# Kernel optimization log

Measured on AMD Instinct MI355X. Metric: run time of the kernel, lower is better.

The kernel has to match this reference:

```python
import jax, jax.numpy as jnp
import numpy as np

WET_MIX = 0.3
FEEDBACK = 0.4
ROOM_SIZE = 0.5
NUM_REFL = 8
NUM_HEADS = 4

# Delay kernel table: int(delay) in {0,1,2,>=3} -> kernel_size {identity,3,5,7}.
# A k-tap kernel with padding k//2 == the same kernel zero-padded to 7 taps with padding 3.
def _gauss7(ks):
    g = np.exp(-np.linspace(-2.0, 2.0, ks) ** 2)
    g = g / g.sum()
    out = np.zeros(7, np.float32)
    s = (7 - ks) // 2
    out[s:s + ks] = g
    return out
_delta = np.zeros(7, np.float32); _delta[3] = 1.0
K_TABLE = jnp.asarray(np.stack([_delta, _gauss7(3), _gauss7(5), _gauss7(7)]))  # [4,7]


def _conv2d(x, w, b, pad):
    y = jax.lax.conv_general_dilated(x, w, (1, 1), [(pad, pad), (pad, pad)],
                                     dimension_numbers=('NCHW', 'OIHW', 'NCHW'))
    return y + b[None, :, None, None]


def _delay_line(x, kern7):
    # vertical depthwise Gaussian blur, same for every (batch, channel) plane
    b, c, h, w = x.shape
    k = kern7.reshape(1, 1, 7, 1)
    y = jax.lax.conv_general_dilated(x.reshape(b * c, 1, h, w), k, (1, 1), [(3, 3), (0, 0)],
                                     dimension_numbers=('NCHW', 'OIHW', 'NCHW'))
    return y.reshape(b, c, h, w)


def _forward(x, refl_w, refl_d, sc_w, sc_b, fb_w, fb_b, d1_w, d1_b, d2_w, d2_b,
             in_proj_w, in_proj_b, out_proj_w, out_proj_b, oc_w, oc_b):
    B, C, H, W = x.shape
    scaled = refl_d * ROOM_SIZE
    kidx = jnp.clip(jnp.floor(scaled).astype(jnp.int32), 0, 3)  # int(delay) detaches grad, as in torch

    wet = jnp.zeros_like(x)
    fb_buf = x * 0.1
    spatial = _conv2d(x, sc_w, sc_b, 1)  # [B,2C,H,W]

    for i in range(NUM_REFL):
        refl = _delay_line(fb_buf, K_TABLE[kidx[i]])
        refl = _conv2d(refl, fb_w, fb_b, 1)
        damp = jax.nn.sigmoid(_conv2d(jax.nn.silu(_conv2d(refl, d1_w, d1_b, 0)), d2_w, d2_b, 0))
        refl = refl * damp
        weight = jax.nn.sigmoid(refl_w[i]) * (0.8 ** i)
        wet = wet + refl * weight
        fb_buf = fb_buf + refl * (FEEDBACK * 0.1)

    # MultiheadAttention over L = H*W tokens, embed_dim=C=4, 4 heads (head_dim=1)
    L = H * W
    hd = C // NUM_HEADS
    wet_flat = wet.reshape(B, C, L).transpose(0, 2, 1)           # [B,L,C]
    qkv = wet_flat @ in_proj_w.T + in_proj_b                     # [B,L,3C]
    q, k, v = jnp.split(qkv, 3, axis=-1)
    def heads(t):
        return t.reshape(B, L, NUM_HEADS, hd).transpose(0, 2, 1, 3)  # [B,H,L,hd]
    q, k, v = heads(q), heads(k), heads(v)
    scores = jnp.einsum('bhqd,bhkd->bhqk', q, k) / np.sqrt(hd).astype(np.float32)
    attn = jax.nn.softmax(scores, axis=-1)
    o = jnp.einsum('bhqk,bhkd->bhqd', attn, v)
    o = o.transpose(0, 2, 1, 3).reshape(B, L, C) @ out_proj_w.T + out_proj_b
    wet2 = o.transpose(0, 2, 1).reshape(B, C, H, W)

    combined = jnp.concatenate([spatial, wet2], axis=1)          # [B,3C,H,W]
    processed_wet = _conv2d(combined, oc_w, oc_b, 0)
    return x * (1.0 - WET_MIX) + processed_wet * WET_MIX


def setup_inputs() -> dict:
    key = jax.random.key(0)
    ks = jax.random.split(key, 16)
    B, C, H, W = 2, 4, 64, 64
    f32 = jnp.float32
    return {
        'x': jax.random.normal(ks[0], (B, C, H, W), f32),
        'refl_w': jax.random.normal(ks[1], (8,), f32) * 0.1,
        'refl_d': jax.random.randint(ks[2], (8,), 1, 16).astype(f32),
        'sc_w': jax.random.normal(ks[3], (2 * C, C, 3, 3), f32) * 0.1,
        'sc_b': jnp.zeros((2 * C,), f32),
        'fb_w': jax.random.normal(ks[4], (C, C, 3, 3), f32) * 0.1,
        'fb_b': jnp.zeros((C,), f32),
        'd1_w': jax.random.normal(ks[5], (C // 2, C, 1, 1), f32) * 0.3,
        'd1_b': jnp.zeros((C // 2,), f32),
        'd2_w': jax.random.normal(ks[6], (C, C // 2, 1, 1), f32) * 0.3,
        'd2_b': jnp.zeros((C,), f32),
        'in_proj_w': jax.random.normal(ks[7], (3 * C, C), f32) * 0.3,
        'in_proj_b': jnp.zeros((3 * C,), f32),
        'out_proj_w': jax.random.normal(ks[8], (C, C), f32) * 0.3,
        'out_proj_b': jnp.zeros((C,), f32),
        'oc_w': jax.random.normal(ks[9], (C, 3 * C, 1, 1), f32) * 0.2,
        'oc_b': jnp.zeros((C,), f32),
    }


def reference(x, refl_w, refl_d, sc_w, sc_b, fb_w, fb_b, d1_w, d1_b, d2_w, d2_b,
              in_proj_w, in_proj_b, out_proj_w, out_proj_b, oc_w, oc_b):
    return _forward(x, refl_w, refl_d, sc_w, sc_b, fb_w, fb_b, d1_w, d1_b, d2_w, d2_b,
                    in_proj_w, in_proj_b, out_proj_w, out_proj_b, oc_w, oc_b)
```

## Files before the change

### kernel.cpp

```cpp
#include <hip/hip_runtime.h>
#include <math.h>


#define ZERO4 make_float4(0.f, 0.f, 0.f, 0.f)

__device__ __forceinline__ float sigf(float v) { return 1.0f / (1.0f + __expf(-v)); }

__device__ __forceinline__ float dppL(float v) {
    return __int_as_float(__builtin_amdgcn_mov_dpp(__float_as_int(v), 0x138, 0xf, 0xf, true));
}
__device__ __forceinline__ float dppR(float v) {
    return __int_as_float(__builtin_amdgcn_mov_dpp(__float_as_int(v), 0x130, 0xf, 0xf, true));
}
__device__ __forceinline__ float4 shL4(float4 v) {
    return make_float4(dppL(v.x), dppL(v.y), dppL(v.z), dppL(v.w));
}
__device__ __forceinline__ float4 shR4(float4 v) {
    return make_float4(dppR(v.x), dppR(v.y), dppR(v.z), dppR(v.w));
}

__device__ __forceinline__ void tapL(float4& a, const float4 t, const float4* w) {
    const float4 w0 = w[0], w1 = w[1], w2 = w[2], w3 = w[3];
    a.x += w0.x * t.x + w1.x * t.y + w2.x * t.z + w3.x * t.w;
    a.y += w0.y * t.x + w1.y * t.y + w2.y * t.z + w3.y * t.w;
    a.z += w0.z * t.x + w1.z * t.y + w2.z * t.z + w3.z * t.w;
    a.w += w0.w * t.x + w1.w * t.y + w2.w * t.z + w3.w * t.w;
}

__global__ __launch_bounds__(1024, 1) void reverb_qkv_kernel(
    const float* __restrict__ x,
    const float* __restrict__ refl_w,
    const float* __restrict__ refl_d,
    const float* __restrict__ fb_w,
    const float* __restrict__ fb_b,
    const float* __restrict__ d1_w,
    const float* __restrict__ d1_b,
    const float* __restrict__ d2_w,
    const float* __restrict__ d2_b,
    const float* __restrict__ ipw,
    const float* __restrict__ ipb,
    float* __restrict__ Qg, float* __restrict__ Kg, float* __restrict__ Vg)
{
    __shared__ float4 P [17 * 64];
    __shared__ float4 BL[17 * 64];
    __shared__ float4 WT[64];
    __shared__ float  GT[3][8];
    __shared__ float  WL[9 * 16];

    const int blk   = blockIdx.x;
    const int batch = blk >> 6;
    const int c0    = blk & 63;
    const int LB    = c0 - 8;
    const int tid   = threadIdx.x;
    const int wy    = tid >> 6;
    const int r     = tid & 63;

    if (tid < 3) {
        const int rr = tid + 1;
        const int ks = 2 * rr + 1;
        const int s  = (7 - ks) >> 1;
        const double step = 4.0 / (double)(ks - 1);
        double g[7]; double sum = 0.0;
        for (int t = 0; t < 7; ++t) {
            if (t < ks) { double u = -2.0 + step * (double)t; g[t] = exp(-u * u); sum += g[t]; }
        }
        for (int t = 0; t < 7; ++t) GT[tid][t] = 0.0f;
        for (int t = 0; t < ks; ++t) GT[tid][s + t] = (float)(g[t] / sum);
    }
    if (tid >= 64 && tid < 64 + 144) {
        const int idx = tid - 64;
        const int oc  = idx / 36;
        const int rem = idx - oc * 36;
        const int ic  = rem / 9;
        const int tp  = rem - ic * 9;
        WL[tp * 16 + ic * 4 + oc] = fb_w[idx];
    }

    for (int idx = tid; idx < 17 * 64; idx += 1024) {
        const int lc  = idx >> 6;
        const int row = idx & 63;
        const int gc  = LB + lc;
        float4 v = ZERO4;
        if (gc >= 0 && gc < 64) {
            const int base = batch * 16384 + row * 64 + gc;
            v.x = 0.1f * x[base];
            v.y = 0.1f * x[base + 4096];
            v.z = 0.1f * x[base + 8192];
            v.w = 0.1f * x[base + 12288];
        }
        P[idx] = v;
    }
    __syncthreads();

    const float4* WL4 = (const float4*)WL;

    double w8 = 1.0;
    for (int j = 0; j < 8; ++j) {
        int kidx = (int)floorf(refl_d[j] * 0.5f);
        kidx = kidx < 0 ? 0 : (kidx > 3 ? 3 : kidx);
        float kv[7];
        #pragma unroll
        for (int u = 0; u < 7; ++u) {
            const float dv = (u == 3) ? 1.0f : 0.0f;
            kv[u] = (kidx == 0) ? dv : GT[kidx - 1][u];
        }
        const float wgt = sigf(refl_w[j]) * (float)w8;

        const int rad = 7 - j;
        const int clo = max(0, c0 - rad);
        const int chi = min(64, c0 + 1 + rad);

        const int lcA   = (clo - 1) - LB;
        const int nBlur = (chi + 1) - (clo - 1);
        for (int t = wy; t < nBlur; t += 16) {
            const int lc = lcA + t;
            const int gc = LB + lc;
            float4 b = ZERO4;
            if (gc >= 0 && gc < 64) {
                const float4 v  = P[lc * 64 + r];
                const float4 l1 = shL4(v),  l2 = shL4(l1), l3 = shL4(l2);
                const float4 r1 = shR4(v),  r2 = shR4(r1), r3 = shR4(r2);
                b.x = kv[0]*l3.x + kv[1]*l2.x + kv[2]*l1.x + kv[3]*v.x
                    + kv[4]*r1.x + kv[5]*r2.x + kv[6]*r3.x;
                b.y = kv[0]*l3.y + kv[1]*l2.y + kv[2]*l1.y + kv[3]*v.y
                    + kv[4]*r1.y + kv[5]*r2.y + kv[6]*r3.y;
                b.z = kv[0]*l3.z + kv[1]*l2.z + kv[2]*l1.z + kv[3]*v.z
                    + kv[4]*r1.z + kv[5]*r2.z + kv[6]*r3.z;
                b.w = kv[0]*l3.w + kv[1]*l2.w + kv[2]*l1.w + kv[3]*v.w
                    + kv[4]*r1.w + kv[5]*r2.w + kv[6]*r3.w;
            }
            BL[lc * 64 + r] = b;
        }
        __syncthreads();

        const int c = clo + wy;
        if (wy < chi - clo) {
            const int lc = c - LB;
            const float4 bm = BL[(lc - 1) * 64 + r];
            const float4 bc = BL[lc * 64 + r];
            const float4 bp = BL[(lc + 1) * 64 + r];

            float4 acc = make_float4(fb_b[0], fb_b[1], fb_b[2], fb_b[3]);
            tapL(acc, shL4(bm), WL4 + 0*4);  tapL(acc, shL4(bc), WL4 + 1*4);  tapL(acc, shL4(bp), WL4 + 2*4);
            tapL(acc, bm,       WL4 + 3*4);  tapL(acc, bc,       WL4 + 4*4);  tapL(acc, bp,       WL4 + 5*4);
            tapL(acc, shR4(bm), WL4 + 6*4);  tapL(acc, shR4(bc), WL4 + 7*4);  tapL(acc, shR4(bp), WL4 + 8*4);

            float4 rr = acc;
            float h0 = d1_b[0] + d1_w[0]*rr.x + d1_w[1]*rr.y + d1_w[2]*rr.z + d1_w[3]*rr.w;
            float h1 = d1_b[1] + d1_w[4]*rr.x + d1_w[5]*rr.y + d1_w[6]*rr.z + d1_w[7]*rr.w;
            h0 = h0 * sigf(h0);
            h1 = h1 * sigf(h1);
            const float d0  = sigf(d2_b[0] + d2_w[0]*h0 + d2_w[1]*h1);
            const float d1v = sigf(d2_b[1] + d2_w[2]*h0 + d2_w[3]*h1);
            const float d2v = sigf(d2_b[2] + d2_w[4]*h0 + d2_w[5]*h1);
            const float d3v = sigf(d2_b[3] + d2_w[6]*h0 + d2_w[7]*h1);
            rr.x *= d0; rr.y *= d1v; rr.z *= d2v; rr.w *= d3v;

            const float4 oldfb = P[lc * 64 + r];
            P[lc * 64 + r] = make_float4(oldfb.x + 0.04f*rr.x, oldfb.y + 0.04f*rr.y,
                                         oldfb.z + 0.04f*rr.z, oldfb.w + 0.04f*rr.w);

            if (c == c0) {
                float4 wv = make_float4(wgt*rr.x, wgt*rr.y, wgt*rr.z, wgt*rr.w);
                if (j > 0) {
                    const float4 old = WT[r];
                    wv.x += old.x; wv.y += old.y; wv.z += old.z; wv.w += old.w;
                }
                WT[r] = wv;
            }
        }
        __syncthreads();
        w8 *= 0.8;
    }

    if (tid < 64) {
        const float4 wv = WT[tid];
        #pragma unroll
        for (int h = 0; h < 4; ++h) {
            const float q = ipb[h]
                + ipw[h*4+0]*wv.x + ipw[h*4+1]*wv.y
                + ipw[h*4+2]*wv.z + ipw[h*4+3]*wv.w;
            const float k = ipb[4+h]
                + ipw[(4+h)*4+0]*wv.x + ipw[(4+h)*4+1]*wv.y
                + ipw[(4+h)*4+2]*wv.z + ipw[(4+h)*4+3]*wv.w;
            const float v = ipb[8+h]
                + ipw[(8+h)*4+0]*wv.x + ipw[(8+h)*4+1]*wv.y
                + ipw[(8+h)*4+2]*wv.z + ipw[(8+h)*4+3]*wv.w;
            const int o = (batch * 4 + h) * 4096 + tid * 64 + c0;
            Qg[o] = q; Kg[o] = k; Vg[o] = v;
        }
    }
}

__global__ __launch_bounds__(512) void attn_kernel(
    const float* __restrict__ Qg, const float* __restrict__ Kg,
    const float* __restrict__ Vg,
    float* __restrict__ PN, float* __restrict__ PD, float* __restrict__ PM)
{
    __shared__ float2 KV[1024];
    __shared__ float  wred[16];
    __shared__ float  pN[4][512], pD[4][512];

    const int bh  = blockIdx.x >> 6;
    const int sub = (blockIdx.x >> 2) & 15;
    const int ks  = blockIdx.x & 3;
    const int tid = threadIdx.x;

    const float* Kp = Kg + bh * 4096 + ks * 1024;
    const float* Vp = Vg + bh * 4096 + ks * 1024;

    float pmax = -3.0e38f, pmin = 3.0e38f;
    #pragma unroll
    for (int t = tid; t < 1024; t += 512) {
        const float kk = Kp[t];
        const float vv = Vp[t];
        KV[t] = make_float2(kk, vv);
        pmax = fmaxf(pmax, kk);
        pmin = fminf(pmin, kk);
    }
    #pragma unroll
    for (int off = 32; off > 0; off >>= 1) {
        pmax = fmaxf(pmax, __shfl_xor(pmax, off, 64));
        pmin = fminf(pmin, __shfl_xor(pmin, off, 64));
    }
    if ((tid & 63) == 0) { wred[tid >> 6] = pmax; wred[8 + (tid >> 6)] = pmin; }
    __syncthreads();
    float kmax = wred[0], kmin = wred[8];
    #pragma unroll
    for (int w = 1; w < 8; ++w) {
        kmax = fmaxf(kmax, wred[w]);
        kmin = fminf(kmin, wred[8 + w]);
    }

    const int ql = tid & 63;
    const int kh = __builtin_amdgcn_readfirstlane(tid >> 6);

    const float L2E = 1.4426950408889634f;
    float q2[4], nm2[4];
    #pragma unroll
    for (int t = 0; t < 4; ++t) {
        const float q = Qg[bh * 4096 + sub * 256 + ql + 64 * t];
        q2[t]  = q * L2E;
        nm2[t] = -(((q >= 0.0f) ? q * kmax : q * kmin) * L2E);
    }

    const float4* KV4 = (const float4*)KV;
    const int base4 = kh * 64;

    float num[4] = {0.f, 0.f, 0.f, 0.f};
    float den[4] = {0.f, 0.f, 0.f, 0.f};
    #pragma unroll 8
    for (int j = 0; j < 64; ++j) {
        const float4 f = KV4[base4 + j];
        #pragma unroll
        for (int t = 0; t < 4; ++t) {
            const float e0 = __builtin_amdgcn_exp2f(__fmaf_rn(q2[t], f.x, nm2[t]));
            den[t] += e0;  num[t] = __fmaf_rn(e0, f.y, num[t]);
            const float e1 = __builtin_amdgcn_exp2f(__fmaf_rn(q2[t], f.z, nm2[t]));
            den[t] += e1;  num[t] = __fmaf_rn(e1, f.w, num[t]);
        }
    }
    #pragma unroll
    for (int t = 0; t < 4; ++t) {
        pN[t][tid] = num[t];
        pD[t][tid] = den[t];
    }
    __syncthreads();
    if (tid < 256) {
        const int which = tid >> 6;
        const int qa    = tid & 63;
        float n = 0.f, d = 0.f;
        #pragma unroll
        for (int w = 0; w < 8; ++w) {
            n += pN[which][w * 64 + qa];
            d += pD[which][w * 64 + qa];
        }
        const int qi = sub * 256 + tid;
        const int o  = bh * 16384 + ks * 4096 + qi;
        PN[o] = n;
        PD[o] = d;
        const float q = Qg[bh * 4096 + qi];
        PM[o] = ((q >= 0.0f) ? q * kmax : q * kmin) * L2E;
    }
}

__global__ __launch_bounds__(128) void final_kernel(
    const float* __restrict__ x,
    const float* __restrict__ sc_w, const float* __restrict__ sc_b,
    const float* __restrict__ opw,  const float* __restrict__ opb,
    const float* __restrict__ ocw,  const float* __restrict__ ocb,
    const float* __restrict__ PN,   const float* __restrict__ PD,
    const float* __restrict__ PM,   float* __restrict__ out)
{
    const int g   = blockIdx.x * 128 + threadIdx.x;
    const int b   = g >> 12;
    const int pix = g & 4095;
    const int y   = pix >> 6;
    const int xc  = pix & 63;

    float xin[4][3][3];
    #pragma unroll
    for (int ic = 0; ic < 4; ++ic)
        #pragma unroll
        for (int ky = 0; ky < 3; ++ky)
            #pragma unroll
            for (int kx = 0; kx < 3; ++kx) {
                const int yy = y + ky - 1, xx = xc + kx - 1;
                xin[ic][ky][kx] = (yy >= 0 && yy < 64 && xx >= 0 && xx < 64)
                                    ? x[(b * 4 + ic) * 4096 + yy * 64 + xx] : 0.f;
            }

    float sp[8];
    #pragma unroll
    for (int oc = 0; oc < 8; ++oc) {
        float a = sc_b[oc];
        #pragma unroll
        for (int ic = 0; ic < 4; ++ic)
            #pragma unroll
            for (int ky = 0; ky < 3; ++ky)
                #pragma unroll
                for (int kx = 0; kx < 3; ++kx)
                    a += sc_w[(oc * 4 + ic) * 9 + ky * 3 + kx] * xin[ic][ky][kx];
        sp[oc] = a;
    }

    float oh[4];
    #pragma unroll
    for (int h = 0; h < 4; ++h) {
        const int bh = b * 4 + h;
        float m2s[4];
        #pragma unroll
        for (int ks = 0; ks < 4; ++ks) m2s[ks] = PM[bh * 16384 + ks * 4096 + pix];
        const float M2 = fmaxf(fmaxf(m2s[0], m2s[1]), fmaxf(m2s[2], m2s[3]));
        float n = 0.f, d = 0.f;
        #pragma unroll
        for (int ks = 0; ks < 4; ++ks) {
            const float s = __builtin_amdgcn_exp2f(m2s[ks] - M2);
            n = __fmaf_rn(PN[bh * 16384 + ks * 4096 + pix], s, n);
            d = __fmaf_rn(PD[bh * 16384 + ks * 4096 + pix], s, d);
        }
        oh[h] = n / d;
    }

    float w2[4];
    #pragma unroll
    for (int c = 0; c < 4; ++c)
        w2[c] = opb[c] + opw[c*4+0]*oh[0] + opw[c*4+1]*oh[1]
                       + opw[c*4+2]*oh[2] + opw[c*4+3]*oh[3];

    #pragma unroll
    for (int c = 0; c < 4; ++c) {
        float a = ocb[c];
        #pragma unroll
        for (int j = 0; j < 8; ++j) a += ocw[c * 12 + j] * sp[j];
        #pragma unroll
        for (int h = 0; h < 4; ++h) a += ocw[c * 12 + 8 + h] * w2[h];
        const int idx = (b * 4 + c) * 4096 + y * 64 + xc;
        out[idx] = 0.7f * x[idx] + 0.3f * a;
    }
}

extern "C" void kernel_launch(void* const* d_in, const int* in_sizes, int n_in,
                              void* d_out, int out_size, void* d_ws, size_t ws_size,
                              hipStream_t stream) {
    const float* x      = (const float*)d_in[0];
    const float* refl_w = (const float*)d_in[1];
    const float* refl_d = (const float*)d_in[2];
    const float* sc_w   = (const float*)d_in[3];
    const float* sc_b   = (const float*)d_in[4];
    const float* fb_w   = (const float*)d_in[5];
    const float* fb_b   = (const float*)d_in[6];
    const float* d1_w   = (const float*)d_in[7];
    const float* d1_b   = (const float*)d_in[8];
    const float* d2_w   = (const float*)d_in[9];
    const float* d2_b   = (const float*)d_in[10];
    const float* ipw    = (const float*)d_in[11];
    const float* ipb    = (const float*)d_in[12];
    const float* opw    = (const float*)d_in[13];
    const float* opb    = (const float*)d_in[14];
    const float* ocw    = (const float*)d_in[15];
    const float* ocb    = (const float*)d_in[16];
    float* out = (float*)d_out;

    float* Q  = (float*)d_ws;
    float* K  = Q + 32768;
    float* V  = K + 32768;
    float* PN = V + 32768;
    float* PD = PN + 131072;
    float* PM = PD + 131072;

    reverb_qkv_kernel<<<dim3(128), dim3(1024), 0, stream>>>(
        x, refl_w, refl_d, fb_w, fb_b, d1_w, d1_b, d2_w, d2_b, ipw, ipb,
        Q, K, V);
    attn_kernel<<<dim3(512), dim3(512), 0, stream>>>(Q, K, V, PN, PD, PM);
    final_kernel<<<dim3(64), dim3(128), 0, stream>>>(
        x, sc_w, sc_b, opw, opb, ocw, ocb, PN, PD, PM, out);
}
```

Baseline: 130.8 us.

## Fuse three kernels into one persistent kernel with grid barriers

```diff
diff --git a/kernel.cpp b/kernel.cpp
--- a/kernel.cpp
+++ b/kernel.cpp
@@ -5,6 +5,26 @@
 #define ZERO4 make_float4(0.f, 0.f, 0.f, 0.f)
 
 __device__ __forceinline__ float sigf(float v) { return 1.0f / (1.0f + __expf(-v)); }
+
+__device__ __forceinline__ float ldA(const float* p) {
+    return __hip_atomic_load(p, __ATOMIC_RELAXED, __HIP_MEMORY_SCOPE_AGENT);
+}
+__device__ __forceinline__ void stA(float* p, float v) {
+    __hip_atomic_store(p, v, __ATOMIC_RELAXED, __HIP_MEMORY_SCOPE_AGENT);
+}
+
+__device__ __forceinline__ void grid_barrier(unsigned* cnt, unsigned target) {
+    __threadfence();
+    __syncthreads();
+    if (threadIdx.x == 0) {
+        __hip_atomic_fetch_add(cnt, 1u, __ATOMIC_ACQ_REL, __HIP_MEMORY_SCOPE_AGENT);
+        while (__hip_atomic_load(cnt, __ATOMIC_RELAXED, __HIP_MEMORY_SCOPE_AGENT) < target) {
+            __builtin_amdgcn_s_sleep(1);
+        }
+    }
+    __syncthreads();
+    __threadfence();
+}
 
 __device__ __forceinline__ float dppL(float v) {
     return __int_as_float(__builtin_amdgcn_mov_dpp(__float_as_int(v), 0x138, 0xf, 0xf, true));
@@ -27,7 +47,7 @@
     a.w += w0.w * t.x + w1.w * t.y + w2.w * t.z + w3.w * t.w;
 }
 
-__global__ __launch_bounds__(1024, 1) void reverb_qkv_kernel(
+__global__ __launch_bounds__(1024, 1) void fused_kernel(
     const float* __restrict__ x,
     const float* __restrict__ refl_w,
     const float* __restrict__ refl_d,
@@ -39,324 +59,341 @@
     const float* __restrict__ d2_b,
     const float* __restrict__ ipw,
     const float* __restrict__ ipb,
-    float* __restrict__ Qg, float* __restrict__ Kg, float* __restrict__ Vg)
+    const float* __restrict__ sc_w, const float* __restrict__ sc_b,
+    const float* __restrict__ opw,  const float* __restrict__ opb,
+    const float* __restrict__ ocw,  const float* __restrict__ ocb,
+    float* Qg, float* Kg, float* Vg,
+    float* PN, float* PD, float* PM,
+    unsigned* bar,
+    float* __restrict__ out)
 {
     __shared__ float4 P [17 * 64];
     __shared__ float4 BL[17 * 64];
     __shared__ float4 WT[64];
     __shared__ float  GT[3][8];
     __shared__ float  WL[9 * 16];
-
-    const int blk   = blockIdx.x;
-    const int batch = blk >> 6;
-    const int c0    = blk & 63;
-    const int LB    = c0 - 8;
-    const int tid   = threadIdx.x;
-    const int wy    = tid >> 6;
-    const int r     = tid & 63;
-
-    if (tid < 3) {
-        const int rr = tid + 1;
-        const int ks = 2 * rr + 1;
-        const int s  = (7 - ks) >> 1;
-        const double step = 4.0 / (double)(ks - 1);
-        double g[7]; double sum = 0.0;
-        for (int t = 0; t < 7; ++t) {
-            if (t < ks) { double u = -2.0 + step * (double)t; g[t] = exp(-u * u); sum += g[t]; }
-        }
-        for (int t = 0; t < 7; ++t) GT[tid][t] = 0.0f;
-        for (int t = 0; t < ks; ++t) GT[tid][s + t] = (float)(g[t] / sum);
+    __shared__ float2 KV2[2048];
+    __shared__ float  wmax[16], wmin[16];
+    __shared__ float  pN[2][4][512], pD[2][4][512];
+
+    const int blk = blockIdx.x;
+    const int tid = threadIdx.x;
+    const int wy  = tid >> 6;
+    const int r   = tid & 63;
+
+    if (blk < 128) {
+        const int batch = blk >> 6;
+        const int c0    = blk & 63;
+        const int LB    = c0 - 8;
+
+        if (tid < 3) {
+            const int rr = tid + 1;
+            const int ks = 2 * rr + 1;
+            const int s  = (7 - ks) >> 1;
+            const double step = 4.0 / (double)(ks - 1);
+            double g[7]; double sum = 0.0;
+            for (int t = 0; t < 7; ++t) {
+                if (t < ks) { double u = -2.0 + step * (double)t; g[t] = exp(-u * u); sum += g[t]; }
+            }
+            for (int t = 0; t < 7; ++t) GT[tid][t] = 0.0f;
+            for (int t = 0; t < ks; ++t) GT[tid][s + t] = (float)(g[t] / sum);
+        }
+        if (tid >= 64 && tid < 64 + 144) {
+            const int idx = tid - 64;
+            const int oc  = idx / 36;
+            const int rem = idx - oc * 36;
+            const int ic  = rem / 9;
+            const int tp  = rem - ic * 9;
+            WL[tp * 16 + ic * 4 + oc] = fb_w[idx];
+        }
+        for (int idx = tid; idx < 17 * 64; idx += 1024) {
+            const int lc  = idx >> 6;
+            const int row = idx & 63;
+            const int gc  = LB + lc;
+            float4 v = ZERO4;
+            if (gc >= 0 && gc < 64) {
+                const int base = batch * 16384 + row * 64 + gc;
+                v.x = 0.1f * x[base];
+                v.y = 0.1f * x[base + 4096];
+                v.z = 0.1f * x[base + 8192];
+                v.w = 0.1f * x[base + 12288];
+            }
+            P[idx] = v;
+        }
+        __syncthreads();
+
+        const float4* WL4 = (const float4*)WL;
+
+        double w8 = 1.0;
+        for (int j = 0; j < 8; ++j) {
+            int kidx = (int)floorf(refl_d[j] * 0.5f);
+            kidx = kidx < 0 ? 0 : (kidx > 3 ? 3 : kidx);
+            float kv[7];
+            #pragma unroll
+            for (int u = 0; u < 7; ++u) {
+                const float dv = (u == 3) ? 1.0f : 0.0f;
+                kv[u] = (kidx == 0) ? dv : GT[kidx - 1][u];
+            }
+            const float wgt = sigf(refl_w[j]) * (float)w8;
+
+            const int rad = 7 - j;
+            const int clo = max(0, c0 - rad);
+            const int chi = min(64, c0 + 1 + rad);
+
+            const int lcA   = (clo - 1) - LB;
+            const int nBlur = (chi + 1) - (clo - 1);
+            for (int t = wy; t < nBlur; t += 16) {
+                const int lc = lcA + t;
+                const int gc = LB + lc;
+                float4 b = ZERO4;
+                if (gc >= 0 && gc < 64) {
+                    const float4 v  = P[lc * 64 + r];
+                    const float4 l1 = shL4(v),  l2 = shL4(l1), l3 = shL4(l2);
+                    const float4 r1 = shR4(v),  r2 = shR4(r1), r3 = shR4(r2);
+                    b.x = kv[0]*l3.x + kv[1]*l2.x + kv[2]*l1.x + kv[3]*v.x
+                        + kv[4]*r1.x + kv[5]*r2.x + kv[6]*r3.x;
+                    b.y = kv[0]*l3.y + kv[1]*l2.y + kv[2]*l1.y + kv[3]*v.y
+                        + kv[4]*r1.y + kv[5]*r2.y + kv[6]*r3.y;
+                    b.z = kv[0]*l3.z + kv[1]*l2.z + kv[2]*l1.z + kv[3]*v.z
+                        + kv[4]*r1.z + kv[5]*r2.z + kv[6]*r3.z;
+                    b.w = kv[0]*l3.w + kv[1]*l2.w + kv[2]*l1.w + kv[3]*v.w
+                        + kv[4]*r1.w + kv[5]*r2.w + kv[6]*r3.w;
+                }
+                BL[lc * 64 + r] = b;
+            }
+            __syncthreads();
+
+            const int c = clo + wy;
+            if (wy < chi - clo) {
+                const int lc = c - LB;
+                const float4 bm = BL[(lc - 1) * 64 + r];
+                const float4 bc = BL[lc * 64 + r];
+                const float4 bp = BL[(lc + 1) * 64 + r];
+
+                float4 acc = make_float4(fb_b[0], fb_b[1], fb_b[2], fb_b[3]);
+                tapL(acc, shL4(bm), WL4 + 0*4);  tapL(acc, shL4(bc), WL4 + 1*4);  tapL(acc, shL4(bp), WL4 + 2*4);
+                tapL(acc, bm,       WL4 + 3*4);  tapL(acc, bc,       WL4 + 4*4);  tapL(acc, bp,       WL4 + 5*4);
+                tapL(acc, shR4(bm), WL4 + 6*4);  tapL(acc, shR4(bc), WL4 + 7*4);  tapL(acc, shR4(bp), WL4 + 8*4);
+
+                float4 rr2 = acc;
+                float h0 = d1_b[0] + d1_w[0]*rr2.x + d1_w[1]*rr2.y + d1_w[2]*rr2.z + d1_w[3]*rr2.w;
+                float h1 = d1_b[1] + d1_w[4]*rr2.x + d1_w[5]*rr2.y + d1_w[6]*rr2.z + d1_w[7]*rr2.w;
+                h0 = h0 * sigf(h0);
+                h1 = h1 * sigf(h1);
+                const float d0  = sigf(d2_b[0] + d2_w[0]*h0 + d2_w[1]*h1);
+                const float d1v = sigf(d2_b[1] + d2_w[2]*h0 + d2_w[3]*h1);
+                const float d2v = sigf(d2_b[2] + d2_w[4]*h0 + d2_w[5]*h1);
+                const float d3v = sigf(d2_b[3] + d2_w[6]*h0 + d2_w[7]*h1);
+                rr2.x *= d0; rr2.y *= d1v; rr2.z *= d2v; rr2.w *= d3v;
+
+                const float4 oldfb = P[lc * 64 + r];
+                P[lc * 64 + r] = make_float4(oldfb.x + 0.04f*rr2.x, oldfb.y + 0.04f*rr2.y,
+                                             oldfb.z + 0.04f*rr2.z, oldfb.w + 0.04f*rr2.w);
+
+                if (c == c0) {
+                    float4 wv = make_float4(wgt*rr2.x, wgt*rr2.y, wgt*rr2.z, wgt*rr2.w);
+                    if (j > 0) {
+                        const float4 old = WT[r];
+                        wv.x += old.x; wv.y += old.y; wv.z += old.z; wv.w += old.w;
+                    }
+                    WT[r] = wv;
+                }
+            }
+            __syncthreads();
+            w8 *= 0.8;
+        }
+
+        if (tid < 64) {
+            const float4 wv = WT[tid];
+            #pragma unroll
+            for (int h = 0; h < 4; ++h) {
+                const float q = ipb[h]
+                    + ipw[h*4+0]*wv.x + ipw[h*4+1]*wv.y
+                    + ipw[h*4+2]*wv.z + ipw[h*4+3]*wv.w;
+                const float k = ipb[4+h]
+                    + ipw[(4+h)*4+0]*wv.x + ipw[(4+h)*4+1]*wv.y
+                    + ipw[(4+h)*4+2]*wv.z + ipw[(4+h)*4+3]*wv.w;
+                const float v = ipb[8+h]
+                    + ipw[(8+h)*4+0]*wv.x + ipw[(8+h)*4+1]*wv.y
+                    + ipw[(8+h)*4+2]*wv.z + ipw[(8+h)*4+3]*wv.w;
+                const int o = (batch * 4 + h) * 4096 + tid * 64 + c0;
+                stA(Qg + o, q); stA(Kg + o, k); stA(Vg + o, v);
+            }
+        }
     }
-    if (tid >= 64 && tid < 64 + 144) {
-        const int idx = tid - 64;
-        const int oc  = idx / 36;
-        const int rem = idx - oc * 36;
-        const int ic  = rem / 9;
-        const int tp  = rem - ic * 9;
-        WL[tp * 16 + ic * 4 + oc] = fb_w[idx];
+
+    grid_barrier(bar, 256u);
+
+    {
+        const int bh = blk >> 5;
+        const int r5 = blk & 31;
+        const int u0 = r5 * 2, u1 = r5 * 2 + 1;
+
+        for (int t = tid; t < 2048; t += 1024) {
+            const int uu   = t >> 10;
+            const int idx  = t & 1023;
+            const int unit = uu ? u1 : u0;
+            const int ksu  = unit & 3;
+            KV2[t] = make_float2(ldA(Kg + bh * 4096 + ksu * 1024 + idx),
+                                 ldA(Vg + bh * 4096 + ksu * 1024 + idx));
+        }
+        __syncthreads();
+
+        const int u   = wy >> 3;
+        const int kh8 = wy & 7;
+        const int unit = u ? u1 : u0;
+        const int sub  = unit >> 2;
+
+        {
+            const int mb = u * 1024 + kh8 * 128 + r;
+            float pmax = fmaxf(KV2[mb].x, KV2[mb + 64].x);
+            float pmin = fminf(KV2[mb].x, KV2[mb + 64].x);
+            #pragma unroll
+            for (int off = 32; off > 0; off >>= 1) {
+                pmax = fmaxf(pmax, __shfl_xor(pmax, off, 64));
+                pmin = fminf(pmin, __shfl_xor(pmin, off, 64));
+            }
+            if (r == 0) { wmax[wy] = pmax; wmin[wy] = pmin; }
+        }
+        __syncthreads();
+        float kmaxU = wmax[u * 8], kminU = wmin[u * 8];
+        #pragma unroll
+        for (int w = 1; w < 8; ++w) {
+            kmaxU = fmaxf(kmaxU, wmax[u * 8 + w]);
+            kminU = fminf(kminU, wmin[u * 8 + w]);
+        }
+
+        const float L2E = 1.4426950408889634f;
+        float q2[4], nm2[4];
+        #pragma unroll
+        for (int t = 0; t < 4; ++t) {
+            const float q = ldA(Qg + bh * 4096 + sub * 256 + r + 64 * t);
+            q2[t]  = q * L2E;
+            nm2[t] = -(((q >= 0.0f) ? q * kmaxU : q * kminU) * L2E);
+        }
+
+        const float4* KV4 = (const float4*)KV2;
+        const int base4 = u * 512 + kh8 * 64;
+
+        float num[4] = {0.f, 0.f, 0.f, 0.f};
+        float den[4] = {0.f, 0.f, 0.f, 0.f};
+        #pragma unroll 8
+        for (int j = 0; j < 64; ++j) {
+            const float4 f = KV4[base4 + j];
+            #pragma unroll
+            for (int t = 0; t < 4; ++t) {
+                const float e0 = __builtin_amdgcn_exp2f(__fmaf_rn(q2[t], f.x, nm2[t]));
+                den[t] += e0;  num[t] = __fmaf_rn(e0, f.y, num[t]);
+                const float e1 = __builtin_amdgcn_exp2f(__fmaf_rn(q2[t], f.z, nm2[t]));
+                den[t] += e1;  num[t] = __fmaf_rn(e1, f.w, num[t]);
+            }
+        }
+        const int windex = kh8 * 64 + r;
+        #pragma unroll
+        for (int t = 0; t < 4; ++t) {
+            pN[u][t][windex] = num[t];
+            pD[u][t][windex] = den[t];
+        }
+        __syncthreads();
+
+        if (tid < 512) {
+            const int ur    = tid >> 8;
+            const int rem   = tid & 255;
+            const int which = rem >> 6;
+            const int qa    = rem & 63;
+            float n = 0.f, d = 0.f;
+            #pragma unroll
+            for (int w = 0; w < 8; ++w) {
+                n += pN[ur][which][w * 64 + qa];
+                d += pD[ur][which][w * 64 + qa];
+            }
+            const int unitr = ur ? u1 : u0;
+            const int subr  = unitr >> 2;
+            const int ksr   = unitr & 3;
+            const int qi    = subr * 256 + which * 64 + qa;
+            const int o     = bh * 16384 + ksr * 4096 + qi;
+            float kmaxR = wmax[ur * 8], kminR = wmin[ur * 8];
+            #pragma unroll
+            for (int w = 1; w < 8; ++w) {
+                kmaxR = fmaxf(kmaxR, wmax[ur * 8 + w]);
+                kminR = fminf(kminR, wmin[ur * 8 + w]);
+            }
+            stA(PN + o, n);
+            stA(PD + o, d);
+            const float q = ldA(Qg + bh * 4096 + qi);
+            stA(PM + o, ((q >= 0.0f) ? q * kmaxR : q * kminR) * L2E);
+        }
     }
 
-    for (int idx = tid; idx < 17 * 64; idx += 1024) {
-        const int lc  = idx >> 6;
-        const int row = idx & 63;
-        const int gc  = LB + lc;
-        float4 v = ZERO4;
-        if (gc >= 0 && gc < 64) {
-            const int base = batch * 16384 + row * 64 + gc;
-            v.x = 0.1f * x[base];
-            v.y = 0.1f * x[base + 4096];
-            v.z = 0.1f * x[base + 8192];
-            v.w = 0.1f * x[base + 12288];
-        }
-        P[idx] = v;
-    }
-    __syncthreads();
-
-    const float4* WL4 = (const float4*)WL;
-
-    double w8 = 1.0;
-    for (int j = 0; j < 8; ++j) {
-        int kidx = (int)floorf(refl_d[j] * 0.5f);
-        kidx = kidx < 0 ? 0 : (kidx > 3 ? 3 : kidx);
-        float kv[7];
-        #pragma unroll
-        for (int u = 0; u < 7; ++u) {
-            const float dv = (u == 3) ? 1.0f : 0.0f;
-            kv[u] = (kidx == 0) ? dv : GT[kidx - 1][u];
-        }
-        const float wgt = sigf(refl_w[j]) * (float)w8;
-
-        const int rad = 7 - j;
-        const int clo = max(0, c0 - rad);
-        const int chi = min(64, c0 + 1 + rad);
-
-        const int lcA   = (clo - 1) - LB;
-        const int nBlur = (chi + 1) - (clo - 1);
-        for (int t = wy; t < nBlur; t += 16) {
-            const int lc = lcA + t;
-            const int gc = LB + lc;
-            float4 b = ZERO4;
-            if (gc >= 0 && gc < 64) {
-                const float4 v  = P[lc * 64 + r];
-                const float4 l1 = shL4(v),  l2 = shL4(l1), l3 = shL4(l2);
-                const float4 r1 = shR4(v),  r2 = shR4(r1), r3 = shR4(r2);
-                b.x = kv[0]*l3.x + kv[1]*l2.x + kv[2]*l1.x + kv[3]*v.x
-                    + kv[4]*r1.x + kv[5]*r2.x + kv[6]*r3.x;
-                b.y = kv[0]*l3.y + kv[1]*l2.y + kv[2]*l1.y + kv[3]*v.y
-                    + kv[4]*r1.y + kv[5]*r2.y + kv[6]*r3.y;
-                b.z = kv[0]*l3.z + kv[1]*l2.z + kv[2]*l1.z + kv[3]*v.z
-                    + kv[4]*r1.z + kv[5]*r2.z + kv[6]*r3.z;
-                b.w = kv[0]*l3.w + kv[1]*l2.w + kv[2]*l1.w + kv[3]*v.w
-                    + kv[4]*r1.w + kv[5]*r2.w + kv[6]*r3.w;
-            }
-            BL[lc * 64 + r] = b;
-        }
-        __syncthreads();
-
-        const int c = clo + wy;
-        if (wy < chi - clo) {
-            const int lc = c - LB;
-            const float4 bm = BL[(lc - 1) * 64 + r];
-            const float4 bc = BL[lc * 64 + r];
-            const float4 bp = BL[(lc + 1) * 64 + r];
-
-            float4 acc = make_float4(fb_b[0], fb_b[1], fb_b[2], fb_b[3]);
-            tapL(acc, shL4(bm), WL4 + 0*4);  tapL(acc, shL4(bc), WL4 + 1*4);  tapL(acc, shL4(bp), WL4 + 2*4);
-            tapL(acc, bm,       WL4 + 3*4);  tapL(acc, bc,       WL4 + 4*4);  tapL(acc, bp,       WL4 + 5*4);
-            tapL(acc, shR4(bm), WL4 + 6*4);  tapL(acc, shR4(bc), WL4 + 7*4);  tapL(acc, shR4(bp), WL4 + 8*4);
-
-            float4 rr = acc;
-            float h0 = d1_b[0] + d1_w[0]*rr.x + d1_w[1]*rr.y + d1_w[2]*rr.z + d1_w[3]*rr.w;
-            float h1 = d1_b[1] + d1_w[4]*rr.x + d1_w[5]*rr.y + d1_w[6]*rr.z + d1_w[7]*rr.w;
-            h0 = h0 * sigf(h0);
-            h1 = h1 * sigf(h1);
-            const float d0  = sigf(d2_b[0] + d2_w[0]*h0 + d2_w[1]*h1);
-            const float d1v = sigf(d2_b[1] + d2_w[2]*h0 + d2_w[3]*h1);
-            const float d2v = sigf(d2_b[2] + d2_w[4]*h0 + d2_w[5]*h1);
-            const float d3v = sigf(d2_b[3] + d2_w[6]*h0 + d2_w[7]*h1);
-            rr.x *= d0; rr.y *= d1v; rr.z *= d2v; rr.w *= d3v;
-
-            const float4 oldfb = P[lc * 64 + r];
-            P[lc * 64 + r] = make_float4(oldfb.x + 0.04f*rr.x, oldfb.y + 0.04f*rr.y,
-                                         oldfb.z + 0.04f*rr.z, oldfb.w + 0.04f*rr.w);
-
-            if (c == c0) {
-                float4 wv = make_float4(wgt*rr.x, wgt*rr.y, wgt*rr.z, wgt*rr.w);
-                if (j > 0) {
-                    const float4 old = WT[r];
-                    wv.x += old.x; wv.y += old.y; wv.z += old.z; wv.w += old.w;
-                }
-                WT[r] = wv;
-            }
-        }
-        __syncthreads();
-        w8 *= 0.8;
-    }
-
-    if (tid < 64) {
-        const float4 wv = WT[tid];
-        #pragma unroll
-        for (int h = 0; h < 4; ++h) {
-            const float q = ipb[h]
-                + ipw[h*4+0]*wv.x + ipw[h*4+1]*wv.y
-                + ipw[h*4+2]*wv.z + ipw[h*4+3]*wv.w;
-            const float k = ipb[4+h]
-                + ipw[(4+h)*4+0]*wv.x + ipw[(4+h)*4+1]*wv.y
-                + ipw[(4+h)*4+2]*wv.z + ipw[(4+h)*4+3]*wv.w;
-            const float v = ipb[8+h]
-                + ipw[(8+h)*4+0]*wv.x + ipw[(8+h)*4+1]*wv.y
-                + ipw[(8+h)*4+2]*wv.z + ipw[(8+h)*4+3]*wv.w;
-            const int o = (batch * 4 + h) * 4096 + tid * 64 + c0;
-            Qg[o] = q; Kg[o] = k; Vg[o] = v;
-        }
-    }
-}
-
-__global__ __launch_bounds__(512) void attn_kernel(
-    const float* __restrict__ Qg, const float* __restrict__ Kg,
-    const float* __restrict__ Vg,
-    float* __restrict__ PN, float* __restrict__ PD, float* __restrict__ PM)
-{
-    __shared__ float2 KV[1024];
-    __shared__ float  wred[16];
-    __shared__ float  pN[4][512], pD[4][512];
-
-    const int bh  = blockIdx.x >> 6;
-    const int sub = (blockIdx.x >> 2) & 15;
-    const int ks  = blockIdx.x & 3;
-    const int tid = threadIdx.x;
-
-    const float* Kp = Kg + bh * 4096 + ks * 1024;
-    const float* Vp = Vg + bh * 4096 + ks * 1024;
-
-    float pmax = -3.0e38f, pmin = 3.0e38f;
-    #pragma unroll
-    for (int t = tid; t < 1024; t += 512) {
-        const float kk = Kp[t];
-        const float vv = Vp[t];
-        KV[t] = make_float2(kk, vv);
-        pmax = fmaxf(pmax, kk);
-        pmin = fminf(pmin, kk);
-    }
-    #pragma unroll
-    for (int off = 32; off > 0; off >>= 1) {
-        pmax = fmaxf(pmax, __shfl_xor(pmax, off, 64));
-        pmin = fminf(pmin, __shfl_xor(pmin, off, 64));
-    }
-    if ((tid & 63) == 0) { wred[tid >> 6] = pmax; wred[8 + (tid >> 6)] = pmin; }
-    __syncthreads();
-    float kmax = wred[0], kmin = wred[8];
-    #pragma unroll
-    for (int w = 1; w < 8; ++w) {
-        kmax = fmaxf(kmax, wred[w]);
-        kmin = fminf(kmin, wred[8 + w]);
-    }
-
-    const int ql = tid & 63;
-    const int kh = __builtin_amdgcn_readfirstlane(tid >> 6);
-
-    const float L2E = 1.4426950408889634f;
-    float q2[4], nm2[4];
-    #pragma unroll
-    for (int t = 0; t < 4; ++t) {
-        const float q = Qg[bh * 4096 + sub * 256 + ql + 64 * t];
-        q2[t]  = q * L2E;
-        nm2[t] = -(((q >= 0.0f) ? q * kmax : q * kmin) * L2E);
-    }
-
-    const float4* KV4 = (const float4*)KV;
-    const int base4 = kh * 64;
-
-    float num[4] = {0.f, 0.f, 0.f, 0.f};
-    float den[4] = {0.f, 0.f, 0.f, 0.f};
-    #pragma unroll 8
-    for (int j = 0; j < 64; ++j) {
-        const float4 f = KV4[base4 + j];
-        #pragma unroll
-        for (int t = 0; t < 4; ++t) {
-            const float e0 = __builtin_amdgcn_exp2f(__fmaf_rn(q2[t], f.x, nm2[t]));
-            den[t] += e0;  num[t] = __fmaf_rn(e0, f.y, num[t]);
-            const float e1 = __builtin_amdgcn_exp2f(__fmaf_rn(q2[t], f.z, nm2[t]));
-            den[t] += e1;  num[t] = __fmaf_rn(e1, f.w, num[t]);
-        }
-    }
-    #pragma unroll
-    for (int t = 0; t < 4; ++t) {
-        pN[t][tid] = num[t];
-        pD[t][tid] = den[t];
-    }
-    __syncthreads();
-    if (tid < 256) {
-        const int which = tid >> 6;
-        const int qa    = tid & 63;
-        float n = 0.f, d = 0.f;
-        #pragma unroll
-        for (int w = 0; w < 8; ++w) {
-            n += pN[which][w * 64 + qa];
-            d += pD[which][w * 64 + qa];
-        }
-        const int qi = sub * 256 + tid;
-        const int o  = bh * 16384 + ks * 4096 + qi;
-        PN[o] = n;
-        PD[o] = d;
-        const float q = Qg[bh * 4096 + qi];
-        PM[o] = ((q >= 0.0f) ? q * kmax : q * kmin) * L2E;
-    }
-}
-
-__global__ __launch_bounds__(128) void final_kernel(
-    const float* __restrict__ x,
-    const float* __restrict__ sc_w, const float* __restrict__ sc_b,
-    const float* __restrict__ opw,  const float* __restrict__ opb,
-    const float* __restrict__ ocw,  const float* __restrict__ ocb,
-    const float* __restrict__ PN,   const float* __restrict__ PD,
-    const float* __restrict__ PM,   float* __restrict__ out)
-{
-    const int g   = blockIdx.x * 128 + threadIdx.x;
-    const int b   = g >> 12;
-    const int pix = g & 4095;
-    const int y   = pix >> 6;
-    const int xc  = pix & 63;
-
-    float xin[4][3][3];
-    #pragma unroll
-    for (int ic = 0; ic < 4; ++ic)
-        #pragma unroll
-        for (int ky = 0; ky < 3; ++ky)
-            #pragma unroll
-            for (int kx = 0; kx < 3; ++kx) {
-                const int yy = y + ky - 1, xx = xc + kx - 1;
-                xin[ic][ky][kx] = (yy >= 0 && yy < 64 && xx >= 0 && xx < 64)
-                                    ? x[(b * 4 + ic) * 4096 + yy * 64 + xx] : 0.f;
-            }
-
-    float sp[8];
-    #pragma unroll
-    for (int oc = 0; oc < 8; ++oc) {
-        float a = sc_b[oc];
+    grid_barrier(bar, 512u);
+
+    if (tid < 32) {
+        const int g   = blk * 32 + tid;
+        const int b   = g >> 12;
+        const int pix = g & 4095;
+        const int y   = pix >> 6;
+        const int xc  = pix & 63;
+
+        float xin[4][3][3];
         #pragma unroll
         for (int ic = 0; ic < 4; ++ic)
             #pragma unroll
             for (int ky = 0; ky < 3; ++ky)
                 #pragma unroll
-                for (int kx = 0; kx < 3; ++kx)
-                    a += sc_w[(oc * 4 + ic) * 9 + ky * 3 + kx] * xin[ic][ky][kx];
-        sp[oc] = a;
-    }
-
-    float oh[4];
-    #pragma unroll
-    for (int h = 0; h < 4; ++h) {
-        const int bh = b * 4 + h;
-        float m2s[4];
-        #pragma unroll
-        for (int ks = 0; ks < 4; ++ks) m2s[ks] = PM[bh * 16384 + ks * 4096 + pix];
-        const float M2 = fmaxf(fmaxf(m2s[0], m2s[1]), fmaxf(m2s[2], m2s[3]));
-        float n = 0.f, d = 0.f;
-        #pragma unroll
-        for (int ks = 0; ks < 4; ++ks) {
-            const float s = __builtin_amdgcn_exp2f(m2s[ks] - M2);
-            n = __fmaf_rn(PN[bh * 16384 + ks * 4096 + pix], s, n);
-            d = __fmaf_rn(PD[bh * 16384 + ks * 4096 + pix], s, d);
-        }
-        oh[h] = n / d;
-    }
-
-    float w2[4];
-    #pragma unroll
-    for (int c = 0; c < 4; ++c)
-        w2[c] = opb[c] + opw[c*4+0]*oh[0] + opw[c*4+1]*oh[1]
-                       + opw[c*4+2]*oh[2] + opw[c*4+3]*oh[3];
-
-    #pragma unroll
-    for (int c = 0; c < 4; ++c) {
-        float a = ocb[c];
-        #pragma unroll
-        for (int j = 0; j < 8; ++j) a += ocw[c * 12 + j] * sp[j];
-        #pragma unroll
-        for (int h = 0; h < 4; ++h) a += ocw[c * 12 + 8 + h] * w2[h];
-        const int idx = (b * 4 + c) * 4096 + y * 64 + xc;
-        out[idx] = 0.7f * x[idx] + 0.3f * a;
+                for (int kx = 0; kx < 3; ++kx) {
+                    const int yy = y + ky - 1, xx = xc + kx - 1;
+                    xin[ic][ky][kx] = (yy >= 0 && yy < 64 && xx >= 0 && xx < 64)
+                                        ? x[(b * 4 + ic) * 4096 + yy * 64 + xx] : 0.f;
+                }
+
+        float sp[8];
+        #pragma unroll
+        for (int oc = 0; oc < 8; ++oc) {
+            float a = sc_b[oc];
+            #pragma unroll
+            for (int ic = 0; ic < 4; ++ic)
+                #pragma unroll
+                for (int ky = 0; ky < 3; ++ky)
+                    #pragma unroll
+                    for (int kx = 0; kx < 3; ++kx)
+                        a += sc_w[(oc * 4 + ic) * 9 + ky * 3 + kx] * xin[ic][ky][kx];
+            sp[oc] = a;
+        }
+
+        float oh[4];
+        #pragma unroll
+        for (int h = 0; h < 4; ++h) {
+            const int bh = b * 4 + h;
+            float m2s[4];
+            #pragma unroll
+            for (int ks = 0; ks < 4; ++ks) m2s[ks] = ldA(PM + bh * 16384 + ks * 4096 + pix);
+            const float M2 = fmaxf(fmaxf(m2s[0], m2s[1]), fmaxf(m2s[2], m2s[3]));
+            float n = 0.f, d = 0.f;
+            #pragma unroll
+            for (int ks = 0; ks < 4; ++ks) {
+                const float s = __builtin_amdgcn_exp2f(m2s[ks] - M2);
+                n = __fmaf_rn(ldA(PN + bh * 16384 + ks * 4096 + pix), s, n);
+                d = __fmaf_rn(ldA(PD + bh * 16384 + ks * 4096 + pix), s, d);
+            }
+            oh[h] = n / d;
+        }
+
+        float w2[4];
+        #pragma unroll
+        for (int c = 0; c < 4; ++c)
+            w2[c] = opb[c] + opw[c*4+0]*oh[0] + opw[c*4+1]*oh[1]
+                           + opw[c*4+2]*oh[2] + opw[c*4+3]*oh[3];
+
+        #pragma unroll
+        for (int c = 0; c < 4; ++c) {
+            float a = ocb[c];
+            #pragma unroll
+            for (int j = 0; j < 8; ++j) a += ocw[c * 12 + j] * sp[j];
+            #pragma unroll
+            for (int h = 0; h < 4; ++h) a += ocw[c * 12 + 8 + h] * w2[h];
+            const int idx = (b * 4 + c) * 4096 + y * 64 + xc;
+            out[idx] = 0.7f * x[idx] + 0.3f * a;
+        }
     }
 }
 
@@ -382,17 +419,18 @@
     const float* ocb    = (const float*)d_in[16];
     float* out = (float*)d_out;
 
-    float* Q  = (float*)d_ws;
-    float* K  = Q + 32768;
-    float* V  = K + 32768;
-    float* PN = V + 32768;
-    float* PD = PN + 131072;
-    float* PM = PD + 131072;
-
-    reverb_qkv_kernel<<<dim3(128), dim3(1024), 0, stream>>>(
+    float*    Q   = (float*)d_ws;
+    float*    K   = Q + 32768;
+    float*    V   = K + 32768;
+    float*    PN  = V + 32768;
+    float*    PD  = PN + 131072;
+    float*    PM  = PD + 131072;
+    unsigned* bar = (unsigned*)(PM + 131072);
+
+    hipMemsetAsync(bar, 0, sizeof(unsigned), stream);
+
+    fused_kernel<<<dim3(256), dim3(1024), 0, stream>>>(
         x, refl_w, refl_d, fb_w, fb_b, d1_w, d1_b, d2_w, d2_b, ipw, ipb,
-        Q, K, V);
-    attn_kernel<<<dim3(512), dim3(512), 0, stream>>>(Q, K, V, PN, PD, PM);
-    final_kernel<<<dim3(64), dim3(128), 0, stream>>>(
-        x, sc_w, sc_b, opw, opb, ocw, ocb, PN, PD, PM, out);
-}
+        sc_w, sc_b, opw, opb, ocw, ocb,
+        Q, K, V, PN, PD, PM, bar, out);
+}
```

Measured after the change: 377.4 us. 2.89x slower.
